# Performance work log

Measured on AMD Instinct MI355X. Metric: run time of the kernel, lower is better.

Reference implementation:

```python
import jax, jax.numpy as jnp
import numpy as np

TAU = 0.02
EPS_NORM = 1e-12  # F.normalize eps


def _l2_normalize(x):
    n = jnp.linalg.norm(x, axis=-1, keepdims=True)
    return x / jnp.maximum(n, EPS_NORM)


def setup_inputs() -> dict:
    key = jax.random.key(0)
    k1, k2, k3, k4 = jax.random.split(key, 4)
    N, D = 8192, 128
    ts_out = jax.random.normal(k1, (N, D), dtype=jnp.float32)
    seq_out = jax.random.normal(k2, (N, D), dtype=jnp.float32)
    omega = jax.random.uniform(k3, (N,), dtype=jnp.float32)  # unused by forward (kept for signature parity)
    patch_mask = jax.random.randint(k4, (N,), 0, 2, dtype=jnp.int32)
    return {"ts_out": ts_out, "seq_out": seq_out, "omega": omega, "patch_mask": patch_mask}


def reference(ts_out, seq_out, omega, patch_mask):
    pm = patch_mask.astype(jnp.float32)              # [N]; detached mask
    patch_sum = pm.sum() + 1e-6
    ts = _l2_normalize(ts_out.reshape(-1, ts_out.shape[-1]))    # [N, D]
    sq = _l2_normalize(seq_out.reshape(-1, seq_out.shape[-1]))  # [N, D]
    logits = jnp.einsum('nd,md->nm', ts, sq) / TAU              # [N, N]
    m = jax.lax.stop_gradient(jnp.max(logits, axis=1, keepdims=True))
    shifted = logits - m                                        # [N, N]
    lse = jnp.log(jnp.sum(jnp.exp(shifted), axis=1))            # [N]
    # masked_omega = eye(N) * patch_mask -> only diagonal entries survive
    diag = jnp.diagonal(shifted)                                # [N]
    log_prob_sum = jnp.sum(pm * (diag - lse))
    return -log_prob_sum / patch_sum
```

## Files before the change

### kernel.cpp

```cpp
#include <hip/hip_runtime.h>
#include <cstdint>
#include <cstddef>

#define N_ROWS 8192
#define DDIM   128
#define K2  72.13475204444817f
#define LN2 0.6931471805599453f
#define NPART 16

typedef _Float16 f16x8 __attribute__((ext_vector_type(8)));
typedef _Float16 f16x4 __attribute__((ext_vector_type(4)));
typedef float    f32x4 __attribute__((ext_vector_type(4)));

typedef const __attribute__((address_space(1))) void GVp;
typedef __attribute__((address_space(3))) void LVp;

__device__ __forceinline__ void gload_lds16(const void* g, void* l) {
  __builtin_amdgcn_global_load_lds((GVp*)g, (LVp*)l, 16, 0, 0);
}

__device__ __forceinline__ float ex2(float x) { return __builtin_amdgcn_exp2f(x); }
__device__ __forceinline__ float lg2(float x) { return __builtin_amdgcn_logf(x); }

__global__ __launch_bounds__(256) void prep(const float* __restrict__ ts,
                                            const float* __restrict__ sq,
                                            _Float16* __restrict__ tsH,
                                            _Float16* __restrict__ sqH,
                                            float* __restrict__ diag2) {
  const int row = blockIdx.x * 8 + (threadIdx.x >> 5);
  const int g   = threadIdx.x & 31;
  const size_t base = (size_t)row * DDIM;

  const float4 a = reinterpret_cast<const float4*>(ts + base)[g];
  const float4 b = reinterpret_cast<const float4*>(sq + base)[g];

  float ssa = a.x * a.x + a.y * a.y + a.z * a.z + a.w * a.w;
  float ssb = b.x * b.x + b.y * b.y + b.z * b.z + b.w * b.w;
  float cr  = a.x * b.x + a.y * b.y + a.z * b.z + a.w * b.w;
  #pragma unroll
  for (int mask = 1; mask <= 16; mask <<= 1) {
    ssa += __shfl_xor(ssa, mask);
    ssb += __shfl_xor(ssb, mask);
    cr  += __shfl_xor(cr,  mask);
  }
  const float ra = 1.0f / fmaxf(sqrtf(ssa), 1e-12f);
  const float rb = 1.0f / fmaxf(sqrtf(ssb), 1e-12f);

  f16x4 ha, hb;
  ha[0] = (_Float16)(a.x * ra); ha[1] = (_Float16)(a.y * ra);
  ha[2] = (_Float16)(a.z * ra); ha[3] = (_Float16)(a.w * ra);
  hb[0] = (_Float16)(b.x * rb); hb[1] = (_Float16)(b.y * rb);
  hb[2] = (_Float16)(b.z * rb); hb[3] = (_Float16)(b.w * rb);
  *reinterpret_cast<f16x4*>(tsH + base + g * 4) = ha;
  *reinterpret_cast<f16x4*>(sqH + base + g * 4) = hb;

  if (g == 0) diag2[row] = cr * ra * rb * K2;
}

__global__ __launch_bounds__(256, 2) void lse16(const _Float16* __restrict__ tsH,
                                                const _Float16* __restrict__ sqH,
                                                float* __restrict__ s_part) {
  __shared__ f16x8 Bl[2][4][8][64];

  const int tid = threadIdx.x;
  const int l   = tid & 63;
  const int wid = tid >> 6;
  const int wr  = wid >> 1;
  const int wc  = wid & 1;
  const int lm  = l & 15;
  const int lk  = l >> 4;

  const int rowbase  = blockIdx.x * 128 + wr * 64;
  const int colbase0 = blockIdx.y * 1024;
  const int sp       = blockIdx.y;

  f16x8 af[4][4];
  #pragma unroll
  for (int ri = 0; ri < 4; ++ri) {
    const size_t arow = (size_t)(rowbase + ri * 16 + lm) * DDIM;
    #pragma unroll
    for (int ks = 0; ks < 4; ++ks)
      af[ri][ks] = *reinterpret_cast<const f16x8*>(tsH + arow + ks * 32 + lk * 8);
  }

  const _Float16* sgp = sqH + (size_t)(colbase0 + lm) * DDIM + wid * 32 + lk * 8;

  f32x4 acc[4][4];
  float sreg[4][4];
  #pragma unroll
  for (int i = 0; i < 4; ++i)
    #pragma unroll
    for (int j = 0; j < 4; ++j) sreg[i][j] = 0.f;

  auto stage = [&](int b, int ct) {
    #pragma unroll
    for (int cg = 0; cg < 8; ++cg)
      gload_lds16(sgp + (size_t)(ct * 128 + cg * 16) * DDIM, &Bl[b][wid][cg][0]);
  };

  stage(0, 0);
  int buf = 0;
  #pragma unroll 1
  for (int ct = 0; ct < 8; ++ct) {
    __syncthreads();
    if (ct < 7) stage(buf ^ 1, ct + 1);

    #pragma unroll
    for (int i = 0; i < 4; ++i)
      #pragma unroll
      for (int j = 0; j < 4; ++j) acc[i][j] = f32x4{0.f, 0.f, 0.f, 0.f};

    #pragma unroll
    for (int ks = 0; ks < 4; ++ks) {
      f16x8 bf[4];
      #pragma unroll
      for (int cj = 0; cj < 4; ++cj) bf[cj] = Bl[buf][ks][wc * 4 + cj][l];
      #pragma unroll
      for (int ri = 0; ri < 4; ++ri)
        #pragma unroll
        for (int cj = 0; cj < 4; ++cj)
          acc[ri][cj] = __builtin_amdgcn_mfma_f32_16x16x32_f16(af[ri][ks], bf[cj],
                                                               acc[ri][cj], 0, 0, 0);
    }

    #pragma unroll
    for (int ri = 0; ri < 4; ++ri)
      #pragma unroll
      for (int r = 0; r < 4; ++r) {
        const float e0 = ex2(fmaf(acc[ri][0][r], K2, -K2));
        const float e1 = ex2(fmaf(acc[ri][1][r], K2, -K2));
        const float e2 = ex2(fmaf(acc[ri][2][r], K2, -K2));
        const float e3 = ex2(fmaf(acc[ri][3][r], K2, -K2));
        sreg[ri][r] += (e0 + e1) + (e2 + e3);
      }
    buf ^= 1;
  }

  #pragma unroll
  for (int ri = 0; ri < 4; ++ri)
    #pragma unroll
    for (int r = 0; r < 4; ++r) {
      float s = sreg[ri][r];
      s += __shfl_xor(s, 1);
      s += __shfl_xor(s, 2);
      s += __shfl_xor(s, 4);
      s += __shfl_xor(s, 8);
      if (lm == 0) {
        const int row = rowbase + ri * 16 + lk * 4 + r;
        s_part[(sp * 2 + wc) * N_ROWS + row] = s;
      }
    }
}

__global__ __launch_bounds__(256) void row_combine(const float* __restrict__ s_part,
                                                   const float* __restrict__ diag2,
                                                   const int* __restrict__ patch_mask,
                                                   float* __restrict__ bp) {
  const int row = blockIdx.x * 256 + threadIdx.x;
  float S = 0.f;
  #pragma unroll
  for (int j = 0; j < NPART; ++j) S += s_part[j * N_ROWS + row];
  const float lse2 = K2 + lg2(fmaxf(S, 1e-37f));
  const float pm   = (float)patch_mask[row];
  float c = pm * LN2 * (diag2[row] - lse2);
  float p = pm;
  #pragma unroll
  for (int mask = 1; mask < 64; mask <<= 1) {
    c += __shfl_xor(c, mask);
    p += __shfl_xor(p, mask);
  }
  __shared__ float rc[4], rp[4];
  const int w = threadIdx.x >> 6;
  if ((threadIdx.x & 63) == 0) { rc[w] = c; rp[w] = p; }
  __syncthreads();
  if (threadIdx.x == 0) {
    bp[blockIdx.x * 2]     = rc[0] + rc[1] + rc[2] + rc[3];
    bp[blockIdx.x * 2 + 1] = rp[0] + rp[1] + rp[2] + rp[3];
  }
}

__global__ __launch_bounds__(64) void finalize(const float* __restrict__ bp,
                                               float* __restrict__ out) {
  const int t = threadIdx.x;
  float c = (t < 32) ? bp[t * 2]     : 0.f;
  float p = (t < 32) ? bp[t * 2 + 1] : 0.f;
  #pragma unroll
  for (int mask = 1; mask < 64; mask <<= 1) {
    c += __shfl_xor(c, mask);
    p += __shfl_xor(p, mask);
  }
  if (t == 0) out[0] = -c / (p + 1e-6f);
}

extern "C" void kernel_launch(void* const* d_in, const int* in_sizes, int n_in,
                              void* d_out, int out_size, void* d_ws, size_t ws_size,
                              hipStream_t stream) {
  const float* ts    = (const float*)d_in[0];
  const float* sq    = (const float*)d_in[1];
  const int*   pmask = (const int*)d_in[3];

  char* w = (char*)d_ws;
  _Float16* tsH    = (_Float16*)w;
  _Float16* sqH    = (_Float16*)(w + (2u << 20));
  float*    diag2  = (float*)(w + (4u << 20));
  float*    s_part = diag2 + N_ROWS;
  float*    bp     = s_part + NPART * N_ROWS;

  prep<<<N_ROWS / 8, 256, 0, stream>>>(ts, sq, tsH, sqH, diag2);
  lse16<<<dim3(64, 8), 256, 0, stream>>>(tsH, sqH, s_part);
  row_combine<<<N_ROWS / 256, 256, 0, stream>>>(s_part, diag2, pmask, bp);
  finalize<<<1, 64, 0, stream>>>(bp, (float*)d_out);
}
```

Before: 94.78 us.

## Fuse row-combine and finalize into lse16 via last-block atomic counters

Folds the row_combine and finalize kernels into the tail of lse16. Per-row-block atomic counters let the last of the 8 column-split blocks reduce its 128 rows, and a global counter lets the last row block write the scalar result. The grid becomes 1D so the 8 column splits of one row block have adjacent block indices, and the counters are zeroed in prep. This removes two kernel launches and their inter-kernel gaps, at the cost of atomics, fences and an extra serial tail on the last blocks.

```diff
diff --git a/kernel.cpp b/kernel.cpp
--- a/kernel.cpp
+++ b/kernel.cpp
@@ -7,6 +7,8 @@
 #define K2  72.13475204444817f
 #define LN2 0.6931471805599453f
 #define NPART 16
+#define NRB   64
+#define NSP   8
 
 typedef _Float16 f16x8 __attribute__((ext_vector_type(8)));
 typedef _Float16 f16x4 __attribute__((ext_vector_type(4)));
@@ -26,7 +28,10 @@
                                             const float* __restrict__ sq,
                                             _Float16* __restrict__ tsH,
                                             _Float16* __restrict__ sqH,
-                                            float* __restrict__ diag2) {
+                                            float* __restrict__ diag2,
+                                            int* __restrict__ counters) {
+  if (blockIdx.x == 0 && threadIdx.x < NRB + 1) counters[threadIdx.x] = 0;
+
   const int row = blockIdx.x * 8 + (threadIdx.x >> 5);
   const int g   = threadIdx.x & 31;
   const size_t base = (size_t)row * DDIM;
@@ -59,7 +64,13 @@
 
 __global__ __launch_bounds__(256, 2) void lse16(const _Float16* __restrict__ tsH,
                                                 const _Float16* __restrict__ sqH,
-                                                float* __restrict__ s_part) {
+                                                float* __restrict__ s_part,
+                                                const float* __restrict__ diag2,
+                                                const int* __restrict__ pmask,
+                                                float* __restrict__ c_rb,
+                                                float* __restrict__ p_rb,
+                                                int* __restrict__ counters,
+                                                float* __restrict__ out) {
   __shared__ f16x8 Bl[2][4][8][64];
 
   const int tid = threadIdx.x;
@@ -70,9 +81,10 @@
   const int lm  = l & 15;
   const int lk  = l >> 4;
 
-  const int rowbase  = blockIdx.x * 128 + wr * 64;
-  const int colbase0 = blockIdx.y * 1024;
-  const int sp       = blockIdx.y;
+  const int rb = (int)blockIdx.x >> 3;
+  const int sp = (int)blockIdx.x & 7;
+  const int rowbase  = rb * 128 + wr * 64;
+  const int colbase0 = sp * 1024;
 
   f16x8 af[4][4];
   #pragma unroll
@@ -150,46 +162,61 @@
         s_part[(sp * 2 + wc) * N_ROWS + row] = s;
       }
     }
-}
-
-__global__ __launch_bounds__(256) void row_combine(const float* __restrict__ s_part,
-                                                   const float* __restrict__ diag2,
-                                                   const int* __restrict__ patch_mask,
-                                                   float* __restrict__ bp) {
-  const int row = blockIdx.x * 256 + threadIdx.x;
-  float S = 0.f;
-  #pragma unroll
-  for (int j = 0; j < NPART; ++j) S += s_part[j * N_ROWS + row];
-  const float lse2 = K2 + lg2(fmaxf(S, 1e-37f));
-  const float pm   = (float)patch_mask[row];
-  float c = pm * LN2 * (diag2[row] - lse2);
-  float p = pm;
+
+  __shared__ int amLastS;
+  __syncthreads();
+  if (tid == 0) {
+    const int old = __hip_atomic_fetch_add(&counters[rb], 1,
+                                           __ATOMIC_ACQ_REL,
+                                           __HIP_MEMORY_SCOPE_AGENT);
+    amLastS = (old == NSP - 1);
+  }
+  __syncthreads();
+  if (!amLastS) return;
+  __threadfence();
+
+  float c = 0.f, p = 0.f;
+  if (tid < 128) {
+    const int row = rb * 128 + tid;
+    float S = 0.f;
+    #pragma unroll
+    for (int j = 0; j < NPART; ++j) S += s_part[j * N_ROWS + row];
+    const float lse2 = K2 + lg2(fmaxf(S, 1e-37f));
+    const float pm   = (float)pmask[row];
+    c = pm * LN2 * (diag2[row] - lse2);
+    p = pm;
+  }
   #pragma unroll
   for (int mask = 1; mask < 64; mask <<= 1) {
     c += __shfl_xor(c, mask);
     p += __shfl_xor(p, mask);
   }
   __shared__ float rc[4], rp[4];
-  const int w = threadIdx.x >> 6;
-  if ((threadIdx.x & 63) == 0) { rc[w] = c; rp[w] = p; }
-  __syncthreads();
-  if (threadIdx.x == 0) {
-    bp[blockIdx.x * 2]     = rc[0] + rc[1] + rc[2] + rc[3];
-    bp[blockIdx.x * 2 + 1] = rp[0] + rp[1] + rp[2] + rp[3];
-  }
-}
-
-__global__ __launch_bounds__(64) void finalize(const float* __restrict__ bp,
-                                               float* __restrict__ out) {
-  const int t = threadIdx.x;
-  float c = (t < 32) ? bp[t * 2]     : 0.f;
-  float p = (t < 32) ? bp[t * 2 + 1] : 0.f;
-  #pragma unroll
-  for (int mask = 1; mask < 64; mask <<= 1) {
-    c += __shfl_xor(c, mask);
-    p += __shfl_xor(p, mask);
-  }
-  if (t == 0) out[0] = -c / (p + 1e-6f);
+  if ((tid & 63) == 0) { rc[tid >> 6] = c; rp[tid >> 6] = p; }
+  __syncthreads();
+  if (tid == 0) {
+    c_rb[rb] = rc[0] + rc[1] + rc[2] + rc[3];
+    p_rb[rb] = rp[0] + rp[1] + rp[2] + rp[3];
+  }
+
+  __shared__ int amFinalS;
+  __syncthreads();
+  if (tid == 0) {
+    const int old = __hip_atomic_fetch_add(&counters[NRB], 1,
+                                           __ATOMIC_ACQ_REL,
+                                           __HIP_MEMORY_SCOPE_AGENT);
+    amFinalS = (old == NRB - 1);
+  }
+  __syncthreads();
+  if (!amFinalS) return;
+  __threadfence();
+
+  if (tid == 0) {
+    float C = 0.f, P = 0.f;
+    #pragma unroll 1
+    for (int i = 0; i < NRB; ++i) { C += c_rb[i]; P += p_rb[i]; }
+    out[0] = -C / (P + 1e-6f);
+  }
 }
 
 extern "C" void kernel_launch(void* const* d_in, const int* in_sizes, int n_in,
@@ -204,10 +231,11 @@
   _Float16* sqH    = (_Float16*)(w + (2u << 20));
   float*    diag2  = (float*)(w + (4u << 20));
   float*    s_part = diag2 + N_ROWS;
-  float*    bp     = s_part + NPART * N_ROWS;
-
-  prep<<<N_ROWS / 8, 256, 0, stream>>>(ts, sq, tsH, sqH, diag2);
-  lse16<<<dim3(64, 8), 256, 0, stream>>>(tsH, sqH, s_part);
-  row_combine<<<N_ROWS / 256, 256, 0, stream>>>(s_part, diag2, pmask, bp);
-  finalize<<<1, 64, 0, stream>>>(bp, (float*)d_out);
-}
+  float*    c_rb   = s_part + NPART * N_ROWS;
+  float*    p_rb   = c_rb + NRB;
+  int*      cnts   = (int*)(p_rb + NRB);
+
+  prep<<<N_ROWS / 8, 256, 0, stream>>>(ts, sq, tsH, sqH, diag2, cnts);
+  lse16<<<NRB * NSP, 256, 0, stream>>>(tsH, sqH, s_part, diag2, pmask,
+                                       c_rb, p_rb, cnts, (float*)d_out);
+}
```

Measured after the change: 129.9 us. 1.37x slower.
